# Kernel tuning notes

Measured on AMD Instinct MI355X. Metric: run time of the kernel, lower is better.

## Reference

```python
import jax, jax.numpy as jnp
import numpy as np
import math

D_MODEL = 64
H = 8
DK = D_MODEL // H


def setup_inputs() -> dict:
    key = jax.random.key(0)
    ks = jax.random.split(key, 6)
    B, C, T, N = 8, D_MODEL, 12, 307
    x = jax.random.normal(ks[0], (B, C, T, N), dtype=jnp.float32)
    mask = jax.random.randint(ks[1], (B, N, N), 0, 2, dtype=jnp.int32)
    s = 1.0 / math.sqrt(D_MODEL)
    Wq = jax.random.uniform(ks[2], (D_MODEL, D_MODEL), jnp.float32, -s, s)
    bq = jax.random.uniform(ks[3], (D_MODEL,), jnp.float32, -s, s)
    Wk = jax.random.uniform(ks[4], (D_MODEL, D_MODEL), jnp.float32, -s, s)
    bk = jax.random.uniform(ks[5], (D_MODEL,), jnp.float32, -s, s)
    return {"x": x, "mask": mask, "Wq": Wq, "bq": bq, "Wk": Wk, "bk": bk}


def reference(x, mask, Wq, bq, Wk, bk):
    # x: [B, d_model, T, N] -> [B, T, N, d_model]
    B, C, T, N = x.shape
    xp = jnp.transpose(x, (0, 2, 3, 1))
    # torch Linear: y = x W^T + b
    q = jnp.einsum('btnd,ed->btne', xp, Wq) + bq
    k = jnp.einsum('btnd,ed->btne', xp, Wk) + bk
    # split heads: [B, T, N, h, dk]
    q = q.reshape(B, T, N, H, DK)
    k = k.reshape(B, T, N, H, DK)
    # QK^T per head then sum over heads (einsum 'ijkmn->ijmn'), fused:
    # scores: [B, T, N, N]
    scores = jnp.einsum('btnhd,btmhd->btnm', q, k) / math.sqrt(DK)
    # mask.unsqueeze(1) -> [B, 1, N, N]
    scores = jnp.where(mask[:, None] == 0, jnp.float32(-1e9), scores)
    # softmax over last dim; dropout is identity in eval mode
    return jax.nn.softmax(scores, axis=-1)
```

## Files before the change

kernel.cpp:

```cpp
#include <hip/hip_runtime.h>
#include <math.h>

#define PB 8
#define PT 12
#define PN 307
#define NP 320
#define SCALE 0.35355339059327373f

typedef short bf16x8 __attribute__((ext_vector_type(8)));
typedef float f32x4  __attribute__((ext_vector_type(4)));
typedef int   i32x4u __attribute__((ext_vector_type(4), aligned(4)));
typedef float f32x4u __attribute__((ext_vector_type(4), aligned(4)));

__device__ __forceinline__ unsigned short f32_to_bf16(float v) {
    unsigned u = __float_as_uint(v);
    u += 0x7FFFu + ((u >> 16) & 1u);
    return (unsigned short)(u >> 16);
}

__device__ __forceinline__ bf16x8 pack8(float4 lo, float4 hi) {
    bf16x8 r;
    r[0] = (short)f32_to_bf16(lo.x); r[1] = (short)f32_to_bf16(lo.y);
    r[2] = (short)f32_to_bf16(lo.z); r[3] = (short)f32_to_bf16(lo.w);
    r[4] = (short)f32_to_bf16(hi.x); r[5] = (short)f32_to_bf16(hi.y);
    r[6] = (short)f32_to_bf16(hi.z); r[7] = (short)f32_to_bf16(hi.w);
    return r;
}

__global__ __launch_bounds__(256) void qk_proj_kernel(
    const float* __restrict__ x,
    const float* __restrict__ Wq, const float* __restrict__ bq,
    const float* __restrict__ Wk, const float* __restrict__ bk,
    unsigned short* __restrict__ qws, unsigned short* __restrict__ kws)
{
    const int tid  = threadIdx.x;
    const int lane = tid & 63;
    const int wv   = tid >> 6;
    const int wn   = wv & 1;
    const int we   = wv >> 1;
    const int chunk = blockIdx.x % 10;
    const int bt    = blockIdx.x / 10;
    const int b = bt / PT, t = bt % PT;
    const int rlo = lane & 15;
    const int kq  = lane >> 4;
    const int n0  = chunk * 32 + wn * 16;

    const int nn = min(n0 + rlo, PN - 1);
    const float* xrow = x + ((size_t)b * 64 * PT + t) * PN + nn;
    bf16x8 a[2];
    #pragma unroll
    for (int ks = 0; ks < 2; ++ks) {
        #pragma unroll
        for (int j = 0; j < 8; ++j) {
            const int c = ks * 32 + kq * 8 + j;
            a[ks][j] = (short)f32_to_bf16(xrow[(size_t)c * PT * PN]);
        }
    }

    f32x4 accq[2] = {}, acck[2] = {};
    #pragma unroll
    for (int eti = 0; eti < 2; ++eti) {
        const int e_row = we * 32 + eti * 16 + rlo;
        const float* wq_r = Wq + (size_t)e_row * 64 + kq * 8;
        const float* wk_r = Wk + (size_t)e_row * 64 + kq * 8;
        #pragma unroll
        for (int ks = 0; ks < 2; ++ks) {
            const bf16x8 bqf = pack8(*(const float4*)(wq_r + ks * 32),
                                     *(const float4*)(wq_r + ks * 32 + 4));
            const bf16x8 bkf = pack8(*(const float4*)(wk_r + ks * 32),
                                     *(const float4*)(wk_r + ks * 32 + 4));
            accq[eti] = __builtin_amdgcn_mfma_f32_16x16x32_bf16(a[ks], bqf, accq[eti], 0, 0, 0);
            acck[eti] = __builtin_amdgcn_mfma_f32_16x16x32_bf16(a[ks], bkf, acck[eti], 0, 0, 0);
        }
    }

    #pragma unroll
    for (int eti = 0; eti < 2; ++eti) {
        const int e = we * 32 + eti * 16 + rlo;
        const float bqv = bq[e], bkv = bk[e];
        #pragma unroll
        for (int r = 0; r < 4; ++r) {
            const int n = n0 + kq * 4 + r;
            if (n < PN) {
                qws[((size_t)bt * NP + n) * 64 + e] = f32_to_bf16(accq[eti][r] + bqv);
                kws[((size_t)bt * NP + n) * 64 + e] = f32_to_bf16(acck[eti][r] + bkv);
            }
        }
    }
}

__global__ __launch_bounds__(256) void attn_kernel(
    const unsigned short* __restrict__ qws,
    const unsigned short* __restrict__ kws,
    const int* __restrict__ mask,
    float* __restrict__ out)
{
    __shared__ float redmx[2][4][16];
    __shared__ float redsm[2][4][16];

    const int tid  = threadIdx.x;
    const int lane = tid & 63;
    const int wm   = tid >> 6;
    const int bid   = blockIdx.x;
    const int ntile = bid % 20;
    const int r2    = bid / 20;
    const int tg    = r2 % 3;
    const int b     = r2 / 3;
    const int ng  = ntile * 16;
    const int nl  = lane & 15;
    const int kq  = lane >> 4;
    const int n   = ng + nl;
    const int nn  = (n < PN) ? n : (PN - 1);

    const int* mrow = mask + ((size_t)b * PN + nn) * PN;
    i32x4u mv[5];
    #pragma unroll
    for (int i = 0; i < 5; ++i)
        mv[i] = *(const i32x4u*)(mrow + (wm * 5 + i) * 16 + kq * 4);

    #pragma unroll 1
    for (int tt = 0; tt < 4; ++tt) {
        const int t  = tg * 4 + tt;
        const int bt = b * PT + t;
        const int p  = tt & 1;

        const bf16x8* qp = (const bf16x8*)(qws + ((size_t)bt * NP + n) * 64 + kq * 8);
        const bf16x8 bq0 = qp[0], bq1 = qp[4];
        const unsigned short* kbase = kws + ((size_t)bt * NP + nl) * 64 + kq * 8;

        f32x4 acc[5] = {};
        #pragma unroll
        for (int i = 0; i < 5; ++i) {
            const int ct = wm * 5 + i;
            const unsigned short* kb = kbase + (size_t)ct * 16 * 64;
            const bf16x8 a0 = *(const bf16x8*)(kb);
            const bf16x8 a1 = *(const bf16x8*)(kb + 32);
            acc[i] = __builtin_amdgcn_mfma_f32_16x16x32_bf16(a0, bq0, acc[i], 0, 0, 0);
            acc[i] = __builtin_amdgcn_mfma_f32_16x16x32_bf16(a1, bq1, acc[i], 0, 0, 0);
        }

        float mx = -INFINITY;
        #pragma unroll
        for (int i = 0; i < 5; ++i) {
            const int ct = wm * 5 + i;
            const int m0 = ct * 16 + kq * 4;
            float sv[4];
            sv[0] = mv[i][0] ? acc[i][0] * SCALE : -1e9f;
            sv[1] = mv[i][1] ? acc[i][1] * SCALE : -1e9f;
            sv[2] = mv[i][2] ? acc[i][2] * SCALE : -1e9f;
            sv[3] = mv[i][3] ? acc[i][3] * SCALE : -1e9f;
            if (ct == 19) {
                #pragma unroll
                for (int r = 0; r < 4; ++r)
                    if (m0 + r >= PN) sv[r] = -INFINITY;
            }
            #pragma unroll
            for (int r = 0; r < 4; ++r) { acc[i][r] = sv[r]; mx = fmaxf(mx, sv[r]); }
        }
        mx = fmaxf(mx, __shfl_xor(mx, 16));
        mx = fmaxf(mx, __shfl_xor(mx, 32));
        if (lane < 16) redmx[p][wm][lane] = mx;
        __syncthreads();
        const float gmx = fmaxf(fmaxf(redmx[p][0][nl], redmx[p][1][nl]),
                                fmaxf(redmx[p][2][nl], redmx[p][3][nl]));

        float sum = 0.f;
        #pragma unroll
        for (int i = 0; i < 5; ++i) {
            #pragma unroll
            for (int r = 0; r < 4; ++r) {
                const float pw = __expf(acc[i][r] - gmx);
                acc[i][r] = pw;
                sum += pw;
            }
        }
        sum += __shfl_xor(sum, 16);
        sum += __shfl_xor(sum, 32);
        if (lane < 16) redsm[p][wm][lane] = sum;
        __syncthreads();
        const float inv = 1.0f / (redsm[p][0][nl] + redsm[p][1][nl] +
                                  redsm[p][2][nl] + redsm[p][3][nl]);

        if (n < PN) {
            float* orow = out + ((size_t)bt * PN + n) * PN;
            #pragma unroll
            for (int i = 0; i < 5; ++i) {
                const int ct = wm * 5 + i;
                const int m0 = ct * 16 + kq * 4;
                if (ct < 19) {
                    f32x4u o;
                    o[0] = acc[i][0] * inv; o[1] = acc[i][1] * inv;
                    o[2] = acc[i][2] * inv; o[3] = acc[i][3] * inv;
                    *(f32x4u*)(orow + m0) = o;
                } else {
                    #pragma unroll
                    for (int r = 0; r < 4; ++r)
                        if (m0 + r < PN) orow[m0 + r] = acc[i][r] * inv;
                }
            }
        }
    }
}

extern "C" void kernel_launch(void* const* d_in, const int* in_sizes, int n_in,
                              void* d_out, int out_size, void* d_ws, size_t ws_size,
                              hipStream_t stream) {
    const float* x  = (const float*)d_in[0];
    const int* mask = (const int*)d_in[1];
    const float* Wq = (const float*)d_in[2];
    const float* bq = (const float*)d_in[3];
    const float* Wk = (const float*)d_in[4];
    const float* bk = (const float*)d_in[5];
    float* out = (float*)d_out;

    unsigned short* qws = (unsigned short*)d_ws;
    unsigned short* kws = qws + (size_t)96 * NP * 64;

    qk_proj_kernel<<<dim3(96 * 10), dim3(256), 0, stream>>>(x, Wq, bq, Wk, bk, qws, kws);
    attn_kernel<<<dim3(8 * 3 * 20), dim3(256), 0, stream>>>(qws, kws, mask, out);
}
```

Baseline: 104.2 us.

## Prefetch next timestep Q/K fragments and merge softmax reductions into one barrier

Loads the Q and K bf16 fragments for the next timestep into registers while the current timestep's softmax runs, and fully unrolls the timestep loop. Each wave now computes its local max and local exp-sum, then exchanges both through shared memory behind a single barrier. The final scale is corrected with exp(local_max - global_max). This removes one __syncthreads per timestep and hides global load latency, at the cost of more registers and a few extra exponentials.

Result: no change. 104.2 us (-0.0%).

```diff
diff --git a/kernel.cpp b/kernel.cpp
--- a/kernel.cpp
+++ b/kernel.cpp
@@ -95,8 +95,7 @@
     const int* __restrict__ mask,
     float* __restrict__ out)
 {
-    __shared__ float redmx[2][4][16];
-    __shared__ float redsm[2][4][16];
+    __shared__ float2 red[2][4][16];
 
     const int tid  = threadIdx.x;
     const int lane = tid & 63;
@@ -118,25 +117,42 @@
     for (int i = 0; i < 5; ++i)
         mv[i] = *(const i32x4u*)(mrow + (wm * 5 + i) * 16 + kq * 4);
 
-    #pragma unroll 1
+    const int bt0 = b * PT + tg * 4;
+    const unsigned short* qb0 = qws + ((size_t)bt0 * NP + n) * 64 + kq * 8;
+    const unsigned short* kb0 = kws + ((size_t)bt0 * NP + nl) * 64 + kq * 8;
+
+    bf16x8 bq0 = *(const bf16x8*)(qb0);
+    bf16x8 bq1 = *(const bf16x8*)(qb0 + 32);
+    bf16x8 ka[5], kb[5];
+    #pragma unroll
+    for (int i = 0; i < 5; ++i) {
+        const unsigned short* kp = kb0 + (size_t)(wm * 5 + i) * 16 * 64;
+        ka[i] = *(const bf16x8*)(kp);
+        kb[i] = *(const bf16x8*)(kp + 32);
+    }
+
+    #pragma unroll
     for (int tt = 0; tt < 4; ++tt) {
-        const int t  = tg * 4 + tt;
-        const int bt = b * PT + t;
+        const int bt = bt0 + tt;
         const int p  = tt & 1;
 
-        const bf16x8* qp = (const bf16x8*)(qws + ((size_t)bt * NP + n) * 64 + kq * 8);
-        const bf16x8 bq0 = qp[0], bq1 = qp[4];
-        const unsigned short* kbase = kws + ((size_t)bt * NP + nl) * 64 + kq * 8;
-
         f32x4 acc[5] = {};
         #pragma unroll
         for (int i = 0; i < 5; ++i) {
-            const int ct = wm * 5 + i;
-            const unsigned short* kb = kbase + (size_t)ct * 16 * 64;
-            const bf16x8 a0 = *(const bf16x8*)(kb);
-            const bf16x8 a1 = *(const bf16x8*)(kb + 32);
-            acc[i] = __builtin_amdgcn_mfma_f32_16x16x32_bf16(a0, bq0, acc[i], 0, 0, 0);
-            acc[i] = __builtin_amdgcn_mfma_f32_16x16x32_bf16(a1, bq1, acc[i], 0, 0, 0);
+            acc[i] = __builtin_amdgcn_mfma_f32_16x16x32_bf16(ka[i], bq0, acc[i], 0, 0, 0);
+            acc[i] = __builtin_amdgcn_mfma_f32_16x16x32_bf16(kb[i], bq1, acc[i], 0, 0, 0);
+        }
+
+        if (tt < 3) {
+            const size_t off = (size_t)(tt + 1) * NP * 64;
+            bq0 = *(const bf16x8*)(qb0 + off);
+            bq1 = *(const bf16x8*)(qb0 + off + 32);
+            #pragma unroll
+            for (int i = 0; i < 5; ++i) {
+                const unsigned short* kp = kb0 + off + (size_t)(wm * 5 + i) * 16 * 64;
+                ka[i] = *(const bf16x8*)(kp);
+                kb[i] = *(const bf16x8*)(kp + 32);
+            }
         }
 
         float mx = -INFINITY;
@@ -159,27 +175,29 @@
         }
         mx = fmaxf(mx, __shfl_xor(mx, 16));
         mx = fmaxf(mx, __shfl_xor(mx, 32));
-        if (lane < 16) redmx[p][wm][lane] = mx;
-        __syncthreads();
-        const float gmx = fmaxf(fmaxf(redmx[p][0][nl], redmx[p][1][nl]),
-                                fmaxf(redmx[p][2][nl], redmx[p][3][nl]));
 
         float sum = 0.f;
         #pragma unroll
         for (int i = 0; i < 5; ++i) {
             #pragma unroll
             for (int r = 0; r < 4; ++r) {
-                const float pw = __expf(acc[i][r] - gmx);
+                const float pw = __expf(acc[i][r] - mx);
                 acc[i][r] = pw;
                 sum += pw;
             }
         }
         sum += __shfl_xor(sum, 16);
         sum += __shfl_xor(sum, 32);
-        if (lane < 16) redsm[p][wm][lane] = sum;
+
+        if (lane < 16) red[p][wm][lane] = make_float2(mx, sum);
         __syncthreads();
-        const float inv = 1.0f / (redsm[p][0][nl] + redsm[p][1][nl] +
-                                  redsm[p][2][nl] + redsm[p][3][nl]);
+
+        const float2 r0 = red[p][0][nl], r1 = red[p][1][nl];
+        const float2 r2v = red[p][2][nl], r3 = red[p][3][nl];
+        const float gmx = fmaxf(fmaxf(r0.x, r1.x), fmaxf(r2v.x, r3.x));
+        const float gsum = r0.y * __expf(r0.x - gmx) + r1.y * __expf(r1.x - gmx)
+                         + r2v.y * __expf(r2v.x - gmx) + r3.y * __expf(r3.x - gmx);
+        const float factor = __expf(mx - gmx) / gsum;
 
         if (n < PN) {
             float* orow = out + ((size_t)bt * PN + n) * PN;
@@ -189,13 +207,13 @@
                 const int m0 = ct * 16 + kq * 4;
                 if (ct < 19) {
                     f32x4u o;
-                    o[0] = acc[i][0] * inv; o[1] = acc[i][1] * inv;
-                    o[2] = acc[i][2] * inv; o[3] = acc[i][3] * inv;
+                    o[0] = acc[i][0] * factor; o[1] = acc[i][1] * factor;
+                    o[2] = acc[i][2] * factor; o[3] = acc[i][3] * factor;
                     *(f32x4u*)(orow + m0) = o;
                 } else {
                     #pragma unroll
                     for (int r = 0; r < 4; ++r)
-                        if (m0 + r < PN) orow[m0 + r] = acc[i][r] * inv;
+                        if (m0 + r < PN) orow[m0 + r] = acc[i][r] * factor;
                 }
             }
         }
```
